# Kernel tuning notes

Measured on AMD Instinct MI355X. Metric: run time of the kernel, lower is better.

Reference implementation:

```python
import jax, jax.numpy as jnp
import numpy as np

H, W = 60, 108          # token grid
WS = 8                  # window size
HEAD = 4
D_MODEL = 512
PAD_B = (WS - H % WS) % WS   # 4
PAD_R = (WS - W % WS) % WS   # 4
NEW_H, NEW_W = H + PAD_B, W + PAD_R
GH, GW = NEW_H // WS, NEW_W // WS


def setup_inputs() -> dict:
    key = jax.random.key(0)
    ks = jax.random.split(key, 9)
    bt, n, c = 16, H * W, D_MODEL
    s = 1.0 / np.sqrt(c)
    return {
        "x": jax.random.normal(ks[0], (bt, n, c), dtype=jnp.float32),
        "t": 4,
        "Wq": jax.random.normal(ks[1], (c, c), dtype=jnp.float32) * s,
        "bq": jnp.zeros((c,), dtype=jnp.float32),
        "Wk": jax.random.normal(ks[2], (c, c), dtype=jnp.float32) * s,
        "bk": jnp.zeros((c,), dtype=jnp.float32),
        "Wv": jax.random.normal(ks[3], (c, c), dtype=jnp.float32) * s,
        "bv": jnp.zeros((c,), dtype=jnp.float32),
        "Wo": jax.random.normal(ks[4], (c, c), dtype=jnp.float32) * s,
        "bo": jnp.zeros((c,), dtype=jnp.float32),
    }


def reference(x, t, Wq, bq, Wk, bk, Wv, bv, Wo, bo):
    bt, n, c = x.shape
    dh = c // HEAD
    # window partition: [bt, H, W, c] -> pad -> [bt, gh*gw, ws*ws, c]
    xg = x.reshape(bt, H, W, c)
    xg = jnp.pad(xg, ((0, 0), (0, PAD_B), (0, PAD_R), (0, 0)))
    xg = xg.reshape(bt, GH, WS, GW, WS, c).transpose(0, 1, 3, 2, 4, 5)
    xg = xg.reshape(bt, GH * GW, WS * WS, c)
    # QKV projections, split heads: [bt, nw, ws2, head, dh]
    q = (xg @ Wq.T + bq).reshape(bt, GH * GW, WS * WS, HEAD, dh)
    k = (xg @ Wk.T + bk).reshape(bt, GH * GW, WS * WS, HEAD, dh)
    v = (xg @ Wv.T + bv).reshape(bt, GH * GW, WS * WS, HEAD, dh)
    scores = jnp.einsum("bwqhd,bwkhd->bwhqk", q, k) / jnp.sqrt(jnp.asarray(dh, x.dtype))
    p = jax.nn.softmax(scores, axis=-1)
    attn = jnp.einsum("bwhqk,bwkhd->bwqhd", p, v)  # [bt, nw, ws2, head, dh]
    # window merge
    y = attn.reshape(bt, GH, GW, WS, WS, c).transpose(0, 1, 3, 2, 4, 5)
    y = y.reshape(bt, NEW_H, NEW_W, c)[:, :H, :W, :].reshape(bt, n, c)
    return y @ Wo.T + bo
```

## Files before the change

kernel.cpp:

```cpp
#include <hip/hip_runtime.h>
#include <hip/hip_bf16.h>

using bf16x8 = __attribute__((ext_vector_type(8))) short;
using f32x4  = __attribute__((ext_vector_type(4))) float;
using u16x4  = __attribute__((ext_vector_type(4))) unsigned short;

constexpr int Ht = 60, Wt = 108, C = 512;
constexpr int GWt = 14, NWIN = 112, NTOK = Ht * Wt, BT = 16;
constexpr int NBLK = BT * NWIN;
constexpr int MROWS = BT * NTOK;
constexpr float SCALE = 0.08838834764831845f;
constexpr size_t WOFF  = 4 * 262144;
constexpr size_t QKVE  = (size_t)MROWS * 1536;
constexpr size_t SLABE = (size_t)NBLK * 64 * 512;

typedef __attribute__((address_space(3))) void lds_void;
typedef const __attribute__((address_space(1))) void g_void;
__device__ __forceinline__ void g2lds16(const void* g, void* l) {
  __builtin_amdgcn_global_load_lds((g_void*)g, (lds_void*)l, 16, 0, 0);
}

__device__ __forceinline__ unsigned short f2b(float f) {
  union { float f; unsigned u; } v; v.f = f;
  unsigned r = v.u + 0x7fffu + ((v.u >> 16) & 1u);
  return (unsigned short)(r >> 16);
}
__device__ __forceinline__ bf16x8 cvt8(float4 a, float4 b) {
  union { bf16x8 v; __hip_bfloat162 h[4]; } u;
  u.h[0] = __float22bfloat162_rn(make_float2(a.x, a.y));
  u.h[1] = __float22bfloat162_rn(make_float2(a.z, a.w));
  u.h[2] = __float22bfloat162_rn(make_float2(b.x, b.y));
  u.h[3] = __float22bfloat162_rn(make_float2(b.z, b.w));
  return u.v;
}

__global__ void cvt_weights(const float* __restrict__ a, const float* __restrict__ b,
                            const float* __restrict__ c, const float* __restrict__ d,
                            unsigned short* __restrict__ dst) {
  int i = blockIdx.x * blockDim.x + threadIdx.x;
  int m  = i >> 16;
  int o4 = i & 65535;
  const float* src = (m == 0) ? a : (m == 1) ? b : (m == 2) ? c : d;
  float4 v = *(const float4*)(src + (size_t)o4 * 4);
  u16x4 o;
  o[0] = f2b(v.x); o[1] = f2b(v.y); o[2] = f2b(v.z); o[3] = f2b(v.w);
  *(u16x4*)(dst + (size_t)m * 262144 + (size_t)o4 * 4) = o;
}

extern "C" __global__ void xcvt_tok(const float* __restrict__ x,
                                    unsigned short* __restrict__ xb) {
  size_t idx = ((size_t)blockIdx.x * 256 + threadIdx.x) * 8;
  float4 a = *(const float4*)(x + idx);
  float4 b = *(const float4*)(x + idx + 4);
  *(bf16x8*)(xb + idx) = cvt8(a, b);
}

extern "C" __global__ __launch_bounds__(256, 4)
void qkv_m97(const unsigned short* __restrict__ xb,
             const unsigned short* __restrict__ wf,
             const float* __restrict__ bq, const float* __restrict__ bk,
             const float* __restrict__ bv,
             unsigned short* __restrict__ qkvs)
{
  __shared__ char As[16384];
  __shared__ char Bs[16384];

  const int tid   = threadIdx.x;
  const int wvid  = tid >> 6;
  const int lane  = tid & 63;
  const int l15   = lane & 15;
  const int rbase = (lane >> 4) << 2;

  const int i    = blockIdx.x;
  const int work = (i & 7) * 1215 + (i >> 3);
  const int t0   = (work / 12) * 128;
  const int j0   = (work % 12) * 128;

  const int lr = lane >> 3;
  const int lc = (lane & 7) ^ lr;
  const unsigned short* gA = xb + (size_t)(t0 + wvid * 32 + lr) * 512 + lc * 8;
  const unsigned short* gB = wf + (size_t)(j0 + wvid * 32 + lr) * 512 + lc * 8;
  char* lA = As + wvid * 4096;
  char* lB = Bs + wvid * 4096;

  f32x4 acc[4][4];
  #pragma unroll
  for (int mt = 0; mt < 4; ++mt)
    #pragma unroll
    for (int nt = 0; nt < 4; ++nt) acc[mt][nt] = (f32x4){0.f, 0.f, 0.f, 0.f};

  const int wr = (wvid >> 1) * 64, wc = (wvid & 1) * 64;

  for (int kk = 0; kk < 512; kk += 64) {
    #pragma unroll
    for (int ii = 0; ii < 4; ++ii) {
      g2lds16(gA + (size_t)ii * 8 * 512 + kk, lA + ii * 1024);
      g2lds16(gB + (size_t)ii * 8 * 512 + kk, lB + ii * 1024);
    }
    __syncthreads();
    #pragma unroll
    for (int ks = 0; ks < 2; ++ks) {
      const int lchunk = ks * 4 + (lane >> 4);
      bf16x8 afr[4], bfr[4];
      #pragma unroll
      for (int mt = 0; mt < 4; ++mt) {
        int row = wr + mt * 16 + l15;
        afr[mt] = *(const bf16x8*)(As + row * 128 + ((lchunk ^ (row & 7)) << 4));
      }
      #pragma unroll
      for (int nt = 0; nt < 4; ++nt) {
        int col = wc + nt * 16 + l15;
        bfr[nt] = *(const bf16x8*)(Bs + col * 128 + ((lchunk ^ (col & 7)) << 4));
      }
      #pragma unroll
      for (int mt = 0; mt < 4; ++mt)
        #pragma unroll
        for (int nt = 0; nt < 4; ++nt)
          acc[mt][nt] = __builtin_amdgcn_mfma_f32_16x16x32_bf16(afr[mt], bfr[nt], acc[mt][nt], 0, 0, 0);
    }
    __syncthreads();
  }

  const int mloc = j0 >> 9;
  const float* bias = (mloc == 0) ? bq : (mloc == 1) ? bk : bv;
  const int jb = j0 & 511;
  #pragma unroll
  for (int nt = 0; nt < 4; ++nt) {
    int col = wc + nt * 16 + l15;
    float bi = bias[jb + col];
    #pragma unroll
    for (int mt = 0; mt < 4; ++mt)
      #pragma unroll
      for (int rg = 0; rg < 4; ++rg) {
        int row = t0 + wr + mt * 16 + rbase + rg;
        qkvs[(size_t)row * 1536 + j0 + col] = f2b(acc[mt][nt][rg] + bi);
      }
  }
}

extern "C" __global__ __launch_bounds__(256, 4)
void attn_tok(unsigned short* __restrict__ qkvs,
              const float* __restrict__ bk, const float* __restrict__ bv)
{
  __shared__ char kbuf[16384];
  __shared__ char vtb[16384];
  __shared__ char pbf[8192];

  const int tid   = threadIdx.x;
  const int wvid  = tid >> 6;
  const int lane  = tid & 63;
  const int l15   = lane & 15;
  const int kl    = (lane >> 4) << 3;
  const int rbase = (lane >> 4) << 2;

  const int w   = blockIdx.x;
  const int h   = blockIdx.y;
  const int b   = w / NWIN;
  const int win = w - b * NWIN;
  const int wy  = win / GWt, wx = win - wy * GWt;
  const int bt0 = b * NTOK;

  auto rowtok = [&](int r, bool& val) {
    int gy = wy * 8 + (r >> 3), gx = wx * 8 + (r & 7);
    val = (gy < Ht) && (gx < Wt);
    return bt0 + gy * Wt + gx;
  };

  #pragma unroll
  for (int it = 0; it < 4; ++it) {
    int f  = it * 256 + tid;
    int r  = f >> 4;
    int c8 = f & 15;
    bool val; int tok = rowtok(r, val);
    bf16x8 v;
    if (val) {
      v = *(const bf16x8*)(qkvs + (size_t)tok * 1536 + 512 + h * 128 + c8 * 8);
    } else {
      #pragma unroll
      for (int e = 0; e < 8; ++e)
        v[e] = (short)f2b(bk[h * 128 + c8 * 8 + e]);
    }
    int off = (r << 8) + (c8 << 4); off ^= (r & 7) << 4;
    *(bf16x8*)(kbuf + off) = v;
  }
  {
    int tok_r = tid & 63;
    int dg    = tid >> 6;
    bool val; int tok = rowtok(tok_r, val);
    bf16x8 vv[4];
    #pragma unroll
    for (int s4 = 0; s4 < 4; ++s4) {
      if (val) {
        vv[s4] = *(const bf16x8*)(qkvs + (size_t)tok * 1536 + 1024 + h * 128 + dg * 32 + s4 * 8);
      } else {
        #pragma unroll
        for (int e = 0; e < 8; ++e)
          vv[s4][e] = (short)f2b(bv[h * 128 + dg * 32 + s4 * 8 + e]);
      }
    }
    #pragma unroll
    for (int s4 = 0; s4 < 4; ++s4)
      #pragma unroll
      for (int e = 0; e < 8; ++e) {
        int d = dg * 32 + s4 * 8 + e;
        int off = (d << 7) + (tok_r << 1); off ^= (d & 7) << 4;
        *(unsigned short*)(vtb + off) = (unsigned short)vv[s4][e];
      }
  }
  __syncthreads();

  int qr = wvid * 16 + l15;
  bool qval; int qtok = rowtok(qr, qval);
  const unsigned short* qrow = qkvs + (size_t)(qval ? qtok : bt0) * 1536 + h * 128;

  f32x4 sacc[4];
  #pragma unroll
  for (int nt = 0; nt < 4; ++nt) sacc[nt] = (f32x4){0.f, 0.f, 0.f, 0.f};
  #pragma unroll
  for (int kk = 0; kk < 128; kk += 32) {
    int ka = kk + kl;
    bf16x8 afr = *(const bf16x8*)(qrow + ka);
    #pragma unroll
    for (int nt = 0; nt < 4; ++nt) {
      int jr = nt * 16 + l15;
      int o2 = (jr << 8) + (ka << 1); o2 ^= (jr & 7) << 4;
      bf16x8 bfr = *(const bf16x8*)(kbuf + o2);
      sacc[nt] = __builtin_amdgcn_mfma_f32_16x16x32_bf16(afr, bfr, sacc[nt], 0, 0, 0);
    }
  }
  #pragma unroll
  for (int rg = 0; rg < 4; ++rg) {
    float mx = -3.0e38f;
    #pragma unroll
    for (int nt = 0; nt < 4; ++nt) mx = fmaxf(mx, sacc[nt][rg]);
    #pragma unroll
    for (int dd = 1; dd < 16; dd <<= 1) mx = fmaxf(mx, __shfl_xor(mx, dd, 64));
    float s = 0.f, e[4];
    #pragma unroll
    for (int nt = 0; nt < 4; ++nt) { e[nt] = __expf((sacc[nt][rg] - mx) * SCALE); s += e[nt]; }
    #pragma unroll
    for (int dd = 1; dd < 16; dd <<= 1) s += __shfl_xor(s, dd, 64);
    float inv = 1.f / s;
    int row = wvid * 16 + rbase + rg;
    #pragma unroll
    for (int nt = 0; nt < 4; ++nt) {
      int col = nt * 16 + l15;
      int off = (row << 7) + (col << 1); off ^= (row & 7) << 4;
      *(unsigned short*)(pbf + off) = f2b(e[nt] * inv);
    }
  }
  __syncthreads();

  f32x4 pacc[4][2];
  #pragma unroll
  for (int mt = 0; mt < 4; ++mt)
    #pragma unroll
    for (int nt = 0; nt < 2; ++nt) pacc[mt][nt] = (f32x4){0.f, 0.f, 0.f, 0.f};
  #pragma unroll
  for (int kk = 0; kk < 64; kk += 32) {
    int ka = kk + kl;
    bf16x8 afr[4];
    #pragma unroll
    for (int mt = 0; mt < 4; ++mt) {
      int row = mt * 16 + l15;
      int off = (row << 7) + (ka << 1); off ^= (row & 7) << 4;
      afr[mt] = *(const bf16x8*)(pbf + off);
    }
    bf16x8 bfr[2];
    #pragma unroll
    for (int nt = 0; nt < 2; ++nt) {
      int d = wvid * 32 + nt * 16 + l15;
      int off = (d << 7) + (ka << 1); off ^= (d & 7) << 4;
      bfr[nt] = *(const bf16x8*)(vtb + off);
    }
    #pragma unroll
    for (int mt = 0; mt < 4; ++mt)
      #pragma unroll
      for (int nt = 0; nt < 2; ++nt)
        pacc[mt][nt] = __builtin_amdgcn_mfma_f32_16x16x32_bf16(afr[mt], bfr[nt], pacc[mt][nt], 0, 0, 0);
  }
  #pragma unroll
  for (int mt = 0; mt < 4; ++mt)
    #pragma unroll
    for (int rg = 0; rg < 4; ++rg) {
      int r = mt * 16 + rbase + rg;
      bool val; int tok = rowtok(r, val);
      if (val) {
        unsigned short* po = qkvs + (size_t)tok * 1536 + h * 128;
        #pragma unroll
        for (int nt = 0; nt < 2; ++nt)
          po[wvid * 32 + nt * 16 + l15] = f2b(pacc[mt][nt][rg]);
      }
    }
}

extern "C" __global__ __launch_bounds__(256, 2)
void proj_tok(const unsigned short* __restrict__ qkvs,
              const unsigned short* __restrict__ wo,
              const float* __restrict__ bo,
              float* __restrict__ out)
{
  __shared__ char smem[65536];
  const int tid   = threadIdx.x;
  const int wvid  = tid >> 6;
  const int lane  = tid & 63;
  const int l15   = lane & 15;
  const int kl    = (lane >> 4) << 3;
  const int rbase = (lane >> 4) << 2;
  const size_t row0 = (size_t)blockIdx.x * 64;

  for (int it = 0; it < 16; ++it) {
    int f  = it * 256 + tid;
    int r  = f >> 6;
    int c8 = f & 63;
    bf16x8 v = *(const bf16x8*)(qkvs + (row0 + r) * 1536 + c8 * 8);
    int off = (r << 10) + (c8 << 4); off ^= (r & 7) << 4;
    *(bf16x8*)(smem + off) = v;
  }
  __syncthreads();

  for (int half = 0; half < 2; ++half) {
    f32x4 acc[4][4];
    #pragma unroll
    for (int mt = 0; mt < 4; ++mt)
      #pragma unroll
      for (int nt = 0; nt < 4; ++nt) acc[mt][nt] = (f32x4){0.f, 0.f, 0.f, 0.f};
    #pragma unroll 2
    for (int kk = 0; kk < 512; kk += 32) {
      int ka = kk + kl;
      bf16x8 afr[4];
      #pragma unroll
      for (int mt = 0; mt < 4; ++mt) {
        int row = mt * 16 + l15;
        int off = (row << 10) + (ka << 1); off ^= (row & 7) << 4;
        afr[mt] = *(const bf16x8*)(smem + off);
      }
      bf16x8 bfr[4];
      #pragma unroll
      for (int nt = 0; nt < 4; ++nt) {
        int j = wvid * 128 + half * 64 + nt * 16 + l15;
        bfr[nt] = *(const bf16x8*)(wo + (size_t)j * 512 + ka);
      }
      #pragma unroll
      for (int mt = 0; mt < 4; ++mt)
        #pragma unroll
        for (int nt = 0; nt < 4; ++nt)
          acc[mt][nt] = __builtin_amdgcn_mfma_f32_16x16x32_bf16(afr[mt], bfr[nt], acc[mt][nt], 0, 0, 0);
    }
    #pragma unroll
    for (int mt = 0; mt < 4; ++mt)
      #pragma unroll
      for (int rg = 0; rg < 4; ++rg) {
        float* po = out + (row0 + mt * 16 + rbase + rg) * 512;
        #pragma unroll
        for (int nt = 0; nt < 4; ++nt) {
          int j = wvid * 128 + half * 64 + nt * 16 + l15;
          po[j] = acc[mt][nt][rg] + bo[j];
        }
      }
  }
}

extern "C" __global__ __launch_bounds__(256, 1)
void qkv_attn(const float* __restrict__ x,
              const unsigned short* __restrict__ wbf,
              const float* __restrict__ bq, const float* __restrict__ bk,
              const float* __restrict__ bv,
              unsigned short* __restrict__ slab)
{
  __shared__ char smem[73728];
  char* qb = smem + 32768;
  char* kb = smem + 49152;
  char* pb = smem + 65536;

  const int tid   = threadIdx.x;
  const int wvid  = tid >> 6;
  const int lane  = tid & 63;
  const int l15   = lane & 15;
  const int kl    = (lane >> 4) << 3;
  const int rbase = (lane >> 4) << 2;

  const int blk = blockIdx.x;
  const int b   = blk / NWIN;
  const int w   = blk - b * NWIN;
  const int wy  = w / GWt, wx = w - wy * GWt;

  for (int it = 0; it < 32; ++it) {
    int f  = it * 256 + tid;
    int r  = f >> 7;
    int c4 = f & 127;
    int gy = wy * 8 + (r >> 3), gx = wx * 8 + (r & 7);
    float4 v = make_float4(0.f, 0.f, 0.f, 0.f);
    if (gy < Ht && gx < Wt)
      v = *(const float4*)(x + ((size_t)b * NTOK + gy * Wt + gx) * C + c4 * 4);
    u16x4 o;
    o[0] = f2b(v.x); o[1] = f2b(v.y); o[2] = f2b(v.z); o[3] = f2b(v.w);
    int lc  = c4 & 63;
    int off = (r << 9) + (lc << 3);
    off ^= (r & 7) << 4;
    off += (c4 >> 6) * 32768;
    *(u16x4*)(smem + off) = o;
  }
  __syncthreads();

  bf16x8 xr[4][8];
  #pragma unroll
  for (int mt = 0; mt < 4; ++mt) {
    int row = mt * 16 + l15;
    #pragma unroll
    for (int s = 0; s < 8; ++s) {
      int off = (row << 9) + ((s * 32 + kl) << 1);
      off ^= (row & 7) << 4;
      xr[mt][s] = *(const bf16x8*)(smem + 32768 + off);
    }
  }
  __syncthreads();

  auto gemm_r = [&](const unsigned short* wm, int h, f32x4 (&acc)[4][2]) {
    #pragma unroll
    for (int mt = 0; mt < 4; ++mt)
      #pragma unroll
      for (int nt = 0; nt < 2; ++nt) acc[mt][nt] = (f32x4){0.f, 0.f, 0.f, 0.f};
    #pragma unroll
    for (int s = 0; s < 16; ++s) {
      int ka = s * 32 + kl;
      bf16x8 afr[4];
      if (s < 8) {
        #pragma unroll
        for (int mt = 0; mt < 4; ++mt) {
          int row = mt * 16 + l15;
          int off = (row << 9) + (ka << 1);
          off ^= (row & 7) << 4;
          afr[mt] = *(const bf16x8*)(smem + off);
        }
      } else {
        #pragma unroll
        for (int mt = 0; mt < 4; ++mt) afr[mt] = xr[mt][s - 8];
      }
      bf16x8 bfr[2];
      #pragma unroll
      for (int nt = 0; nt < 2; ++nt) {
        int jg = h * 128 + wvid * 32 + nt * 16 + l15;
        bfr[nt] = *(const bf16x8*)(wm + (size_t)jg * 512 + ka);
      }
      #pragma unroll
      for (int mt = 0; mt < 4; ++mt)
        #pragma unroll
        for (int nt = 0; nt < 2; ++nt)
          acc[mt][nt] = __builtin_amdgcn_mfma_f32_16x16x32_bf16(afr[mt], bfr[nt], acc[mt][nt], 0, 0, 0);
    }
  };

  auto store_rm = [&](f32x4 (&acc)[4][2], char* base, const float* bias, int h) {
    #pragma unroll
    for (int nt = 0; nt < 2; ++nt) {
      int col = wvid * 32 + nt * 16 + l15;
      float bi = bias[h * 128 + col];
      #pragma unroll
      for (int mt = 0; mt < 4; ++mt)
        #pragma unroll
        for (int rg = 0; rg < 4; ++rg) {
          int row = mt * 16 + rbase + rg;
          int off = (row << 8) + (col << 1);
          off ^= (row & 7) << 4;
          *(unsigned short*)(base + off) = f2b(acc[mt][nt][rg] + bi);
        }
    }
  };

  unsigned short* sl = slab + (size_t)blk * 32768;

  for (int h = 0; h < 4; ++h) {
    {
      f32x4 acc[4][2];
      gemm_r(wbf + 0 * 262144, h, acc);
      store_rm(acc, qb, bq, h);
      gemm_r(wbf + 1 * 262144, h, acc);
      store_rm(acc, kb, bk, h);
    }
    __syncthreads();
    f32x4 vacc[4][2];
    {
      f32x4 sacc[4];
      #pragma unroll
      for (int nt = 0; nt < 4; ++nt) sacc[nt] = (f32x4){0.f, 0.f, 0.f, 0.f};
      #pragma unroll
      for (int kk = 0; kk < 128; kk += 32) {
        int ka = kk + kl;
        int row = wvid * 16 + l15;
        int off = (row << 8) + (ka << 1); off ^= (row & 7) << 4;
        bf16x8 afr = *(const bf16x8*)(qb + off);
        #pragma unroll
        for (int nt = 0; nt < 4; ++nt) {
          int jr = nt * 16 + l15;
          int o2 = (jr << 8) + (ka << 1); o2 ^= (jr & 7) << 4;
          bf16x8 bfr = *(const bf16x8*)(kb + o2);
          sacc[nt] = __builtin_amdgcn_mfma_f32_16x16x32_bf16(afr, bfr, sacc[nt], 0, 0, 0);
        }
      }
      #pragma unroll
      for (int rg = 0; rg < 4; ++rg) {
        float mx = -3.0e38f;
        #pragma unroll
        for (int nt = 0; nt < 4; ++nt) mx = fmaxf(mx, sacc[nt][rg]);
        #pragma unroll
        for (int dd = 1; dd < 16; dd <<= 1) mx = fmaxf(mx, __shfl_xor(mx, dd, 64));
        float s = 0.f, e[4];
        #pragma unroll
        for (int nt = 0; nt < 4; ++nt) { e[nt] = __expf((sacc[nt][rg] - mx) * SCALE); s += e[nt]; }
        #pragma unroll
        for (int dd = 1; dd < 16; dd <<= 1) s += __shfl_xor(s, dd, 64);
        float inv = 1.f / s;
        int row = wvid * 16 + rbase + rg;
        #pragma unroll
        for (int nt = 0; nt < 4; ++nt) {
          int col = nt * 16 + l15;
          int off = (row << 7) + (col << 1); off ^= (row & 7) << 4;
          *(unsigned short*)(pb + off) = f2b(e[nt] * inv);
        }
      }
      gemm_r(wbf + 2 * 262144, h, vacc);
    }
    __syncthreads();
    {
      #pragma unroll
      for (int nt = 0; nt < 2; ++nt) {
        int d = wvid * 32 + nt * 16 + l15;
        float bi = bv[h * 128 + d];
        #pragma unroll
        for (int mt = 0; mt < 4; ++mt) {
          int j0 = mt * 16 + rbase;
          u16x4 pk;
          #pragma unroll
          for (int rg = 0; rg < 4; ++rg) pk[rg] = f2b(vacc[mt][nt][rg] + bi);
          int off = (d << 7) + (j0 << 1); off ^= (d & 7) << 4;
          *(u16x4*)(kb + off) = pk;
        }
      }
    }
    __syncthreads();
    {
      f32x4 pacc[4][2];
      #pragma unroll
      for (int mt = 0; mt < 4; ++mt)
        #pragma unroll
        for (int nt = 0; nt < 2; ++nt) pacc[mt][nt] = (f32x4){0.f, 0.f, 0.f, 0.f};
      #pragma unroll
      for (int kk = 0; kk < 64; kk += 32) {
        int ka = kk + kl;
        bf16x8 afr[4];
        #pragma unroll
        for (int mt = 0; mt < 4; ++mt) {
          int row = mt * 16 + l15;
          int off = (row << 7) + (ka << 1); off ^= (row & 7) << 4;
          afr[mt] = *(const bf16x8*)(pb + off);
        }
        bf16x8 bfr[2];
        #pragma unroll
        for (int nt = 0; nt < 2; ++nt) {
          int d = wvid * 32 + nt * 16 + l15;
          int off = (d << 7) + (ka << 1); off ^= (d & 7) << 4;
          bfr[nt] = *(const bf16x8*)(kb + off);
        }
        #pragma unroll
        for (int mt = 0; mt < 4; ++mt)
          #pragma unroll
          for (int nt = 0; nt < 2; ++nt)
            pacc[mt][nt] = __builtin_amdgcn_mfma_f32_16x16x32_bf16(afr[mt], bfr[nt], pacc[mt][nt], 0, 0, 0);
      }
      #pragma unroll
      for (int nt = 0; nt < 2; ++nt) {
        int d = wvid * 32 + nt * 16 + l15;
        #pragma unroll
        for (int mt = 0; mt < 4; ++mt)
          #pragma unroll
          for (int rg = 0; rg < 4; ++rg) {
            int row = mt * 16 + rbase + rg;
            sl[row * 512 + h * 128 + d] = f2b(pacc[mt][nt][rg]);
          }
      }
    }
    __syncthreads();
  }
}

extern "C" __global__ __launch_bounds__(256, 2)
void proj_win(const unsigned short* __restrict__ slab,
              const unsigned short* __restrict__ wo,
              const float* __restrict__ bo,
              float* __restrict__ out)
{
  __shared__ char smem[65536];
  const int tid   = threadIdx.x;
  const int wvid  = tid >> 6;
  const int lane  = tid & 63;
  const int l15   = lane & 15;
  const int kl    = (lane >> 4) << 3;
  const int rbase = (lane >> 4) << 2;

  const int blk = blockIdx.x;
  const int b   = blk / NWIN;
  const int w   = blk - b * NWIN;
  const int wy  = w / GWt, wx = w - wy * GWt;

  const unsigned short* src = slab + (size_t)blk * 32768;
  for (int it = 0; it < 16; ++it) {
    int f  = it * 256 + tid;
    int r  = f >> 6;
    int c8 = f & 63;
    bf16x8 v = *(const bf16x8*)(src + r * 512 + c8 * 8);
    int off = (r << 10) + (c8 << 4);
    off ^= (r & 7) << 4;
    *(bf16x8*)(smem + off) = v;
  }
  __syncthreads();

  for (int half = 0; half < 2; ++half) {
    f32x4 acc[4][4];
    #pragma unroll
    for (int mt = 0; mt < 4; ++mt)
      #pragma unroll
      for (int nt = 0; nt < 4; ++nt) acc[mt][nt] = (f32x4){0.f, 0.f, 0.f, 0.f};
    #pragma unroll 2
    for (int kk = 0; kk < 512; kk += 32) {
      int ka = kk + kl;
      bf16x8 afr[4];
      #pragma unroll
      for (int mt = 0; mt < 4; ++mt) {
        int row = mt * 16 + l15;
        int off = (row << 10) + (ka << 1); off ^= (row & 7) << 4;
        afr[mt] = *(const bf16x8*)(smem + off);
      }
      bf16x8 bfr[4];
      #pragma unroll
      for (int nt = 0; nt < 4; ++nt) {
        int j = wvid * 128 + half * 64 + nt * 16 + l15;
        bfr[nt] = *(const bf16x8*)(wo + (size_t)j * 512 + ka);
      }
      #pragma unroll
      for (int mt = 0; mt < 4; ++mt)
        #pragma unroll
        for (int nt = 0; nt < 4; ++nt)
          acc[mt][nt] = __builtin_amdgcn_mfma_f32_16x16x32_bf16(afr[mt], bfr[nt], acc[mt][nt], 0, 0, 0);
    }
    #pragma unroll
    for (int mt = 0; mt < 4; ++mt)
      #pragma unroll
      for (int rg = 0; rg < 4; ++rg) {
        int r = mt * 16 + rbase + rg;
        int gy = wy * 8 + (r >> 3), gx = wx * 8 + (r & 7);
        if (gy < Ht && gx < Wt) {
          float* po = out + ((size_t)b * NTOK + gy * Wt + gx) * C;
          #pragma unroll
          for (int nt = 0; nt < 4; ++nt) {
            int j = wvid * 128 + half * 64 + nt * 16 + l15;
            po[j] = acc[mt][nt][rg] + bo[j];
          }
        }
      }
  }
}

extern "C" void kernel_launch(void* const* d_in, const int* in_sizes, int n_in,
                              void* d_out, int out_size, void* d_ws, size_t ws_size,
                              hipStream_t stream) {
  const float* x  = (const float*)d_in[0];
  const float* Wq = (const float*)d_in[2];
  const float* bq = (const float*)d_in[3];
  const float* Wk = (const float*)d_in[4];
  const float* bk = (const float*)d_in[5];
  const float* Wv = (const float*)d_in[6];
  const float* bv = (const float*)d_in[7];
  const float* Wo = (const float*)d_in[8];
  const float* bo = (const float*)d_in[9];
  unsigned short* wbf = (unsigned short*)d_ws;

  cvt_weights<<<1024, 256, 0, stream>>>(Wq, Wk, Wv, Wo, wbf);

  const size_t need_full = (WOFF + QKVE) * 2;
  const size_t need_r7   = (WOFF + SLABE) * 2;

  if (ws_size >= need_full) {
    unsigned short* qkvs = wbf + WOFF;
    unsigned short* xb   = (unsigned short*)d_out;
    xcvt_tok<<<MROWS * 512 / 2048, 256, 0, stream>>>(x, xb);
    qkv_m97<<<9720, 256, 0, stream>>>(xb, wbf, bq, bk, bv, qkvs);
    attn_tok<<<dim3(NBLK, 4), 256, 0, stream>>>(qkvs, bk, bv);
    proj_tok<<<MROWS / 64, 256, 0, stream>>>(qkvs, wbf + 3 * 262144, bo, (float*)d_out);
  } else if (ws_size >= need_r7) {
    unsigned short* slab = wbf + WOFF;
    qkv_attn<<<NBLK, 256, 0, stream>>>(x, wbf, bq, bk, bv, slab);
    proj_win<<<NBLK, 256, 0, stream>>>(slab, wbf + 3 * 262144, bo, (float*)d_out);
  }
}
```

Baseline: 534.5 us.

## Stage Q tile in LDS for attention and retile output projection GEMM

The attention kernel now loads Q for the window into LDS alongside K, and reuses that buffer for the probability matrix, instead of reading Q fragments straight from global memory. The output projection is replaced by a 128x128-tiled GEMM that stages both the activations and Wo through LDS with direct global-to-LDS loads and a swizzled layout, with a remapped block order. The old projection read Wo fragments directly from global for every k-step. The trade-offs are an extra barrier in the attention kernel, more LDS per block there (occupancy hint lowered from 4 to 3), and a new tile schedule for the projection.

```diff
diff --git a/kernel.cpp b/kernel.cpp
--- a/kernel.cpp
+++ b/kernel.cpp
@@ -138,13 +138,13 @@
   }
 }
 
-extern "C" __global__ __launch_bounds__(256, 4)
+extern "C" __global__ __launch_bounds__(256, 3)
 void attn_tok(unsigned short* __restrict__ qkvs,
               const float* __restrict__ bk, const float* __restrict__ bv)
 {
   __shared__ char kbuf[16384];
   __shared__ char vtb[16384];
-  __shared__ char pbf[8192];
+  __shared__ char qpb[16384];
 
   const int tid   = threadIdx.x;
   const int wvid  = tid >> 6;
@@ -172,16 +172,21 @@
     int r  = f >> 4;
     int c8 = f & 15;
     bool val; int tok = rowtok(r, val);
-    bf16x8 v;
+    int off = (r << 8) + (c8 << 4); off ^= (r & 7) << 4;
+    bf16x8 q, k;
     if (val) {
-      v = *(const bf16x8*)(qkvs + (size_t)tok * 1536 + 512 + h * 128 + c8 * 8);
+      const unsigned short* base = qkvs + (size_t)tok * 1536 + h * 128 + c8 * 8;
+      q = *(const bf16x8*)(base);
+      k = *(const bf16x8*)(base + 512);
     } else {
       #pragma unroll
-      for (int e = 0; e < 8; ++e)
-        v[e] = (short)f2b(bk[h * 128 + c8 * 8 + e]);
-    }
-    int off = (r << 8) + (c8 << 4); off ^= (r & 7) << 4;
-    *(bf16x8*)(kbuf + off) = v;
+      for (int e = 0; e < 8; ++e) {
+        q[e] = 0;
+        k[e] = (short)f2b(bk[h * 128 + c8 * 8 + e]);
+      }
+    }
+    *(bf16x8*)(qpb + off) = q;
+    *(bf16x8*)(kbuf + off) = k;
   }
   {
     int tok_r = tid & 63;
@@ -209,17 +214,15 @@
   }
   __syncthreads();
 
-  int qr = wvid * 16 + l15;
-  bool qval; int qtok = rowtok(qr, qval);
-  const unsigned short* qrow = qkvs + (size_t)(qval ? qtok : bt0) * 1536 + h * 128;
-
   f32x4 sacc[4];
   #pragma unroll
   for (int nt = 0; nt < 4; ++nt) sacc[nt] = (f32x4){0.f, 0.f, 0.f, 0.f};
   #pragma unroll
   for (int kk = 0; kk < 128; kk += 32) {
     int ka = kk + kl;
-    bf16x8 afr = *(const bf16x8*)(qrow + ka);
+    int qr = wvid * 16 + l15;
+    int qo = (qr << 8) + (ka << 1); qo ^= (qr & 7) << 4;
+    bf16x8 afr = *(const bf16x8*)(qpb + qo);
     #pragma unroll
     for (int nt = 0; nt < 4; ++nt) {
       int jr = nt * 16 + l15;
@@ -228,6 +231,8 @@
       sacc[nt] = __builtin_amdgcn_mfma_f32_16x16x32_bf16(afr, bfr, sacc[nt], 0, 0, 0);
     }
   }
+  __syncthreads();
+
   #pragma unroll
   for (int rg = 0; rg < 4; ++rg) {
     float mx = -3.0e38f;
@@ -246,7 +251,7 @@
     for (int nt = 0; nt < 4; ++nt) {
       int col = nt * 16 + l15;
       int off = (row << 7) + (col << 1); off ^= (row & 7) << 4;
-      *(unsigned short*)(pbf + off) = f2b(e[nt] * inv);
+      *(unsigned short*)(qpb + off) = f2b(e[nt] * inv);
     }
   }
   __syncthreads();
@@ -264,7 +269,7 @@
     for (int mt = 0; mt < 4; ++mt) {
       int row = mt * 16 + l15;
       int off = (row << 7) + (ka << 1); off ^= (row & 7) << 4;
-      afr[mt] = *(const bf16x8*)(pbf + off);
+      afr[mt] = *(const bf16x8*)(qpb + off);
     }
     bf16x8 bfr[2];
     #pragma unroll
@@ -294,52 +299,61 @@
     }
 }
 
-extern "C" __global__ __launch_bounds__(256, 2)
-void proj_tok(const unsigned short* __restrict__ qkvs,
+extern "C" __global__ __launch_bounds__(256, 4)
+void proj_m97(const unsigned short* __restrict__ qkvs,
               const unsigned short* __restrict__ wo,
               const float* __restrict__ bo,
               float* __restrict__ out)
 {
-  __shared__ char smem[65536];
+  __shared__ char As[16384];
+  __shared__ char Bs[16384];
+
   const int tid   = threadIdx.x;
   const int wvid  = tid >> 6;
   const int lane  = tid & 63;
   const int l15   = lane & 15;
-  const int kl    = (lane >> 4) << 3;
   const int rbase = (lane >> 4) << 2;
-  const size_t row0 = (size_t)blockIdx.x * 64;
-
-  for (int it = 0; it < 16; ++it) {
-    int f  = it * 256 + tid;
-    int r  = f >> 6;
-    int c8 = f & 63;
-    bf16x8 v = *(const bf16x8*)(qkvs + (row0 + r) * 1536 + c8 * 8);
-    int off = (r << 10) + (c8 << 4); off ^= (r & 7) << 4;
-    *(bf16x8*)(smem + off) = v;
-  }
-  __syncthreads();
-
-  for (int half = 0; half < 2; ++half) {
-    f32x4 acc[4][4];
-    #pragma unroll
-    for (int mt = 0; mt < 4; ++mt)
-      #pragma unroll
-      for (int nt = 0; nt < 4; ++nt) acc[mt][nt] = (f32x4){0.f, 0.f, 0.f, 0.f};
-    #pragma unroll 2
-    for (int kk = 0; kk < 512; kk += 32) {
-      int ka = kk + kl;
-      bf16x8 afr[4];
+
+  const int i    = blockIdx.x;
+  const int work = (i & 7) * 405 + (i >> 3);
+  const int t0   = (work >> 2) * 128;
+  const int j0   = (work & 3) * 128;
+
+  const int lr = lane >> 3;
+  const int lc = (lane & 7) ^ lr;
+  const unsigned short* gA = qkvs + (size_t)(t0 + wvid * 32 + lr) * 1536 + lc * 8;
+  const unsigned short* gB = wo + (size_t)(j0 + wvid * 32 + lr) * 512 + lc * 8;
+  char* lA = As + wvid * 4096;
+  char* lB = Bs + wvid * 4096;
+
+  f32x4 acc[4][4];
+  #pragma unroll
+  for (int mt = 0; mt < 4; ++mt)
+    #pragma unroll
+    for (int nt = 0; nt < 4; ++nt) acc[mt][nt] = (f32x4){0.f, 0.f, 0.f, 0.f};
+
+  const int wr = (wvid >> 1) * 64, wc = (wvid & 1) * 64;
+
+  for (int kk = 0; kk < 512; kk += 64) {
+    #pragma unroll
+    for (int ii = 0; ii < 4; ++ii) {
+      g2lds16(gA + (size_t)ii * 8 * 1536 + kk, lA + ii * 1024);
+      g2lds16(gB + (size_t)ii * 8 * 512 + kk, lB + ii * 1024);
+    }
+    __syncthreads();
+    #pragma unroll
+    for (int ks = 0; ks < 2; ++ks) {
+      const int lchunk = ks * 4 + (lane >> 4);
+      bf16x8 afr[4], bfr[4];
       #pragma unroll
       for (int mt = 0; mt < 4; ++mt) {
-        int row = mt * 16 + l15;
-        int off = (row << 10) + (ka << 1); off ^= (row & 7) << 4;
-        afr[mt] = *(const bf16x8*)(smem + off);
-      }
-      bf16x8 bfr[4];
+        int row = wr + mt * 16 + l15;
+        afr[mt] = *(const bf16x8*)(As + row * 128 + ((lchunk ^ (row & 7)) << 4));
+      }
       #pragma unroll
       for (int nt = 0; nt < 4; ++nt) {
-        int j = wvid * 128 + half * 64 + nt * 16 + l15;
-        bfr[nt] = *(const bf16x8*)(wo + (size_t)j * 512 + ka);
+        int col = wc + nt * 16 + l15;
+        bfr[nt] = *(const bf16x8*)(Bs + col * 128 + ((lchunk ^ (col & 7)) << 4));
       }
       #pragma unroll
       for (int mt = 0; mt < 4; ++mt)
@@ -347,16 +361,19 @@
         for (int nt = 0; nt < 4; ++nt)
           acc[mt][nt] = __builtin_amdgcn_mfma_f32_16x16x32_bf16(afr[mt], bfr[nt], acc[mt][nt], 0, 0, 0);
     }
+    __syncthreads();
+  }
+
+  #pragma unroll
+  for (int nt = 0; nt < 4; ++nt) {
+    int col = j0 + wc + nt * 16 + l15;
+    float bi = bo[col];
     #pragma unroll
     for (int mt = 0; mt < 4; ++mt)
       #pragma unroll
       for (int rg = 0; rg < 4; ++rg) {
-        float* po = out + (row0 + mt * 16 + rbase + rg) * 512;
-        #pragma unroll
-        for (int nt = 0; nt < 4; ++nt) {
-          int j = wvid * 128 + half * 64 + nt * 16 + l15;
-          po[j] = acc[mt][nt][rg] + bo[j];
-        }
+        int row = t0 + wr + mt * 16 + rbase + rg;
+        out[(size_t)row * 512 + col] = acc[mt][nt][rg] + bi;
       }
   }
 }
@@ -686,7 +703,7 @@
     xcvt_tok<<<MROWS * 512 / 2048, 256, 0, stream>>>(x, xb);
     qkv_m97<<<9720, 256, 0, stream>>>(xb, wbf, bq, bk, bv, qkvs);
     attn_tok<<<dim3(NBLK, 4), 256, 0, stream>>>(qkvs, bk, bv);
-    proj_tok<<<MROWS / 64, 256, 0, stream>>>(qkvs, wbf + 3 * 262144, bo, (float*)d_out);
+    proj_m97<<<3240, 256, 0, stream>>>(qkvs, wbf + 3 * 262144, bo, (float*)d_out);
   } else if (ws_size >= need_r7) {
     unsigned short* slab = wbf + WOFF;
     qkv_attn<<<NBLK, 256, 0, stream>>>(x, wbf, bq, bk, bv, slab);
```

After: 498.6 us (median of 2 runs). 6.7% less time.
